# Kernel tuning notes

Hardware: AMD Instinct MI355X
Metric: run time of the kernel (lower is better)

Reference implementation:

```python
import jax, jax.numpy as jnp
import numpy as np

B, N, DIM, VDIM, H, HD = 4, 1369, 1024, 1536, 16, 64
ROPE_HW, ROPE_DIM, THETA = 37, 32, 10000.0
LN_EPS = 1e-5


def _rope_tables():
    # VisionRotaryEmbeddingFast: freqs_for='lang', dim=32, pt_seq_len=ft_seq_len=37
    inv = 1.0 / THETA ** (jnp.arange(0, ROPE_DIM, 2, dtype=jnp.float32) / ROPE_DIM)  # [16]
    t = jnp.arange(ROPE_HW, dtype=jnp.float32) / ROPE_HW * ROPE_HW                    # [37]
    f = t[:, None] * inv[None, :]                                                     # [37,16]
    f = jnp.repeat(f, 2, axis=-1)                                                     # [37,32]
    # broadcat along last dim over the 2D grid -> [37,37,64]
    f2 = jnp.concatenate([jnp.broadcast_to(f[:, None, :], (ROPE_HW, ROPE_HW, ROPE_DIM)),
                          jnp.broadcast_to(f[None, :, :], (ROPE_HW, ROPE_HW, ROPE_DIM))], axis=-1)
    f2 = f2.reshape(-1, 2 * ROPE_DIM)                                                 # [1369,64]
    return jnp.cos(f2), jnp.sin(f2)


def _rotate_half(x):
    # pairs (x0,x1) -> (-x1,x0), interleaved
    xr = x.reshape(*x.shape[:-1], x.shape[-1] // 2, 2)
    x1, x2 = xr[..., 0], xr[..., 1]
    return jnp.stack((-x2, x1), axis=-1).reshape(x.shape)


def setup_inputs() -> dict:
    key = jax.random.key(0)
    ks = jax.random.split(key, 8)
    return {
        "x": jax.random.normal(ks[0], (B, N, DIM), jnp.float32),
        "value": jax.random.normal(ks[1], (B, N, VDIM), jnp.float32),
        "attn_mask": jax.random.randint(ks[2], (B, N), 0, 2).astype(bool),
        "wq": jax.random.normal(ks[3], (DIM, DIM), jnp.float32) * 0.02,
        "wk": jax.random.normal(ks[4], (DIM, VDIM), jnp.float32) * 0.02,
        "wv": jax.random.normal(ks[5], (DIM, VDIM), jnp.float32) * 0.02,
        "ln_g": jnp.ones((DIM,), jnp.float32),
        "ln_b": jnp.zeros((DIM,), jnp.float32),
        "wp": jax.random.normal(ks[6], (DIM, DIM), jnp.float32) * 0.02,
        "bp": jnp.zeros((DIM,), jnp.float32),
    }


def reference(x, value, attn_mask, wq, wk, wv, ln_g, ln_b, wp, bp):
    cos, sin = _rope_tables()  # [N, 64] each
    # projections (torch F.linear: y = x @ W.T)
    q = jnp.einsum('bni,oi->bno', x, wq).reshape(B, N, H, HD).transpose(0, 2, 1, 3)
    k = jnp.einsum('bni,oi->bno', value, wk).reshape(B, N, H, HD).transpose(0, 2, 1, 3)
    v = jnp.einsum('bni,oi->bno', value, wv).reshape(B, N, H, HD).transpose(0, 2, 1, 3)
    # inline RoPE on q and k
    q = q * cos + _rotate_half(q) * sin
    k = k * cos + _rotate_half(k) * sin
    q = q * (HD ** -0.5)
    attn = jnp.einsum('bhnd,bhmd->bhnm', q, k)
    neg_inf = jnp.finfo(attn.dtype).min
    attn = jnp.where(attn_mask[:, None, None, :], attn, neg_inf)
    attn = jax.nn.softmax(attn, axis=-1)
    out = jnp.einsum('bhnm,bhmd->bhnd', attn, v)
    out = out.transpose(0, 2, 1, 3).reshape(B, N, H * HD)
    # inner_attn_ln (LayerNorm, eps=1e-5)
    mu = jnp.mean(out, axis=-1, keepdims=True)
    var = jnp.var(out, axis=-1, keepdims=True)
    out = (out - mu) * jax.lax.rsqrt(var + LN_EPS) * ln_g + ln_b
    # output projection
    return jnp.einsum('bni,oi->bno', out, wp) + bp
```

## Files before the change

kernel.cpp:

```cpp
#include <hip/hip_runtime.h>
#include <hip/hip_bf16.h>

#define BB 4
#define NN 1369
#define DIMM 1024
#define VDIMM 1536
#define HH 16
#define MM (BB*NN)
#define MPAD 5504
#define MPAD2 5632
#define NPAD 1408
#define KVB 64
#define NT (NPAD/KVB)
#define NT2 (NPAD/128)
#define QSCALE 0.18028334f

typedef __attribute__((ext_vector_type(4))) float f32x4;
typedef __attribute__((ext_vector_type(8))) __bf16 bf16x8;
typedef __attribute__((ext_vector_type(4))) __bf16 bf16x4;

#define GLOAD_LDS(gsrc, ldst) \
  __builtin_amdgcn_global_load_lds((const __attribute__((address_space(1))) unsigned int*)(gsrc), \
                                   (__attribute__((address_space(3))) unsigned int*)(ldst), 16, 0, 0)

__global__ __launch_bounds__(256) void cvt_inputs(const float* __restrict__ x,
                                                  const float* __restrict__ val,
                                                  __bf16* __restrict__ xb,
                                                  __bf16* __restrict__ vb) {
  const int NX = MM * 1024 / 4;
  const int NV = MM * 1536 / 4;
  int i = blockIdx.x * blockDim.x + threadIdx.x;
  int st = gridDim.x * blockDim.x;
  for (; i < NX + NV; i += st) {
    const float* s; __bf16* d; int j;
    if (i < NX) { s = x; d = xb; j = i; }
    else        { s = val; d = vb; j = i - NX; }
    f32x4 v = ((const f32x4*)s)[j];
    bf16x4 o;
    o[0] = (__bf16)v[0]; o[1] = (__bf16)v[1];
    o[2] = (__bf16)v[2]; o[3] = (__bf16)v[3];
    ((bf16x4*)d)[j] = o;
  }
}

__global__ __launch_bounds__(256) void cvt_weights(
    const float* __restrict__ wq, const float* __restrict__ wk,
    const float* __restrict__ wv, const float* __restrict__ wp,
    const float* __restrict__ g,
    __bf16* __restrict__ wqb, __bf16* __restrict__ wkvb, __bf16* __restrict__ wgb) {
  const int NQ = 1024 * 1024 / 4;
  const int NK = 1024 * 1536 / 4;
  int i = blockIdx.x * blockDim.x + threadIdx.x;
  int st = gridDim.x * blockDim.x;
  for (; i < 2 * NQ + 2 * NK; i += st) {
    int j = i;
    if (j < NQ) {
      f32x4 v = ((const f32x4*)wq)[j];
      bf16x4 o;
      o[0] = (__bf16)v[0]; o[1] = (__bf16)v[1]; o[2] = (__bf16)v[2]; o[3] = (__bf16)v[3];
      ((bf16x4*)wqb)[j] = o;
    } else if (j < NQ + NK) {
      j -= NQ;
      f32x4 v = ((const f32x4*)wk)[j];
      bf16x4 o;
      o[0] = (__bf16)v[0]; o[1] = (__bf16)v[1]; o[2] = (__bf16)v[2]; o[3] = (__bf16)v[3];
      ((bf16x4*)wkvb)[j] = o;
    } else if (j < NQ + 2 * NK) {
      j -= NQ + NK;
      f32x4 v = ((const f32x4*)wv)[j];
      bf16x4 o;
      o[0] = (__bf16)v[0]; o[1] = (__bf16)v[1]; o[2] = (__bf16)v[2]; o[3] = (__bf16)v[3];
      ((bf16x4*)(wkvb + (size_t)1024 * 1536))[j] = o;
    } else {
      j -= NQ + 2 * NK;
      f32x4 v = ((const f32x4*)wp)[j];
      f32x4 gv = ((const f32x4*)g)[j & 255];
      bf16x4 o;
      o[0] = (__bf16)(v[0] * gv[0]); o[1] = (__bf16)(v[1] * gv[1]);
      o[2] = (__bf16)(v[2] * gv[2]); o[3] = (__bf16)(v[3] * gv[3]);
      ((bf16x4*)wgb)[j] = o;
    }
  }
}

__global__ __launch_bounds__(256) void c12_kernel(
    const float* __restrict__ wp, const float* __restrict__ g,
    const float* __restrict__ lnb, const float* __restrict__ bpv,
    float* __restrict__ c1, float* __restrict__ c2) {
  const int w = threadIdx.x >> 6, l = threadIdx.x & 63;
  const int o = blockIdx.x * 4 + w;
  const float* row = wp + (size_t)o * 1024;
  float s1 = 0.f, s2 = 0.f;
#pragma unroll
  for (int j = 0; j < 4; ++j) {
    const int idx = l * 4 + j * 256;
    f32x4 wv = *(const f32x4*)&row[idx];
    f32x4 gv = *(const f32x4*)&g[idx];
    f32x4 bv = *(const f32x4*)&lnb[idx];
#pragma unroll
    for (int e = 0; e < 4; ++e) { s1 += wv[e] * gv[e]; s2 += wv[e] * bv[e]; }
  }
#pragma unroll
  for (int m = 1; m < 64; m <<= 1) { s1 += __shfl_xor(s1, m); s2 += __shfl_xor(s2, m); }
  if (l == 0) { c1[o] = s1; c2[o] = s2 + bpv[o]; }
}

__global__ __launch_bounds__(256) void stats_kernel(
    const __bf16* __restrict__ AO, float* __restrict__ mu, float* __restrict__ rstd) {
  const int w = threadIdx.x >> 6, l = threadIdx.x & 63;
  const int row = blockIdx.x * 4 + w;
  const __bf16* x = AO + (size_t)row * DIMM + l * 16;
  float s = 0.f, sq = 0.f;
#pragma unroll
  for (int j = 0; j < 2; ++j) {
    bf16x8 v = *(const bf16x8*)&x[j * 8];
#pragma unroll
    for (int e = 0; e < 8; ++e) { float f = (float)v[e]; s += f; sq += f * f; }
  }
#pragma unroll
  for (int m = 1; m < 64; m <<= 1) { s += __shfl_xor(s, m); sq += __shfl_xor(sq, m); }
  if (l == 0) {
    float mean = s * (1.f / 1024.f);
    mu[row] = mean;
    rstd[row] = rsqrtf(sq * (1.f / 1024.f) - mean * mean + 1e-5f);
  }
}

__global__ __launch_bounds__(256) void prep_aux(float* __restrict__ cosT,
                                                float* __restrict__ sinT,
                                                const void* __restrict__ mask,
                                                float* __restrict__ maskA) {
  const int blk = blockIdx.x;
  if (blk < 343) {
    int idx = blk * 256 + threadIdx.x;
    if (idx >= NN * 64) return;
    int n = idx >> 6, d = idx & 63;
    int r = n / 37, c = n % 37;
    int m = (d < 32) ? (d >> 1) : ((d - 32) >> 1);
    float p = (d < 32) ? (float)r : (float)c;
    float inv = powf(10000.f, -(float)m * (1.f / 16.f));
    float a = p * inv;
    cosT[idx] = cosf(a);
    sinT[idx] = sinf(a);
  } else {
    __shared__ int flags[2];
    int t = threadIdx.x;
    if (t < 2) flags[t] = 0;
    __syncthreads();
    const unsigned int* mw = (const unsigned int*)mask;
    for (int i = t; i < NN; i += blockDim.x) {
      unsigned int w = mw[i];
      if (w == 0x3F800000u) atomicOr(&flags[1], 1);
      else if (w > 1u) atomicOr(&flags[0], 1);
    }
    __syncthreads();
    int md = flags[1] ? 2 : (flags[0] ? 1 : 0);
    const unsigned char* mb = (const unsigned char*)mask;
    const float* mf = (const float*)mask;
    for (int i = t; i < BB * NPAD; i += blockDim.x) {
      int b = i / NPAD, key = i % NPAD;
      float v = -1e30f;
      if (key < NN) {
        int idx = b * NN + key;
        bool on = (md == 0) ? (mw[idx] != 0u) : (md == 1) ? (mb[idx] != 0) : (mf[idx] != 0.f);
        if (on) v = 0.f;
      }
      maskA[i] = v;
    }
  }
}

__global__ __launch_bounds__(512, 2) void gemm_kv256(
    const __bf16* __restrict__ A, const __bf16* __restrict__ W,
    __bf16* __restrict__ Kb, __bf16* __restrict__ Vtb,
    const float* __restrict__ cosT, const float* __restrict__ sinT) {
  __shared__ __bf16 Ar[4][256 * 32];
  __shared__ __bf16 Br[4][256 * 32];
  const int tid = threadIdx.x;
  const int wid = tid >> 6, l = tid & 63;
  const int wr = wid >> 2, wc = wid & 3;
  const int lo = l & 15, hi = l >> 4;
  const int tN = blockIdx.x & 7, tM = blockIdx.x >> 3;
  const int K = VDIMM;
  const int nk = K / 32;

  const int srow = (tid >> 6) * 16 + (tid & 15);
  const int schunk = ((tid >> 4) & 3) * 8;
  const __bf16* Asrc = A + (size_t)(tM * 256 + srow) * K + schunk;
  const __bf16* Wsrc = W + (size_t)(tN * 256 + srow) * K + schunk;

  f32x4 zero = {0.f, 0.f, 0.f, 0.f};
  f32x4 acc[8][4];
#pragma unroll
  for (int i = 0; i < 8; ++i)
#pragma unroll
    for (int j = 0; j < 4; ++j) acc[i][j] = zero;

  auto GSTAGE = [&](int s, int k0) {
    GLOAD_LDS(Asrc + k0,                   (char*)&Ar[s][0] + tid * 16);
    GLOAD_LDS(Asrc + (size_t)128 * K + k0, (char*)&Ar[s][0] + tid * 16 + 8192);
    GLOAD_LDS(Wsrc + k0,                   (char*)&Br[s][0] + tid * 16);
    GLOAD_LDS(Wsrc + (size_t)128 * K + k0, (char*)&Br[s][0] + tid * 16 + 8192);
  };

  GSTAGE(0, 0);
  GSTAGE(1, 32);
  for (int t = 0; t < nk; ++t) {
    if (t < nk - 1) asm volatile("s_waitcnt vmcnt(4)" ::: "memory");
    else            asm volatile("s_waitcnt vmcnt(0)" ::: "memory");
    __builtin_amdgcn_s_barrier();
    const int s = t & 3;
    bf16x8 af[8], bf[4];
#pragma unroll
    for (int mi = 0; mi < 8; ++mi)
      af[mi] = *(const bf16x8*)&Ar[s][(wr * 8 + mi) * 512 + hi * 128 + lo * 8];
#pragma unroll
    for (int ni = 0; ni < 4; ++ni)
      bf[ni] = *(const bf16x8*)&Br[s][(wc * 4 + ni) * 512 + hi * 128 + lo * 8];
    if (t + 2 < nk) GSTAGE((t + 2) & 3, (t + 2) * 32);
    __builtin_amdgcn_s_setprio(1);
#pragma unroll
    for (int mi = 0; mi < 8; ++mi)
#pragma unroll
      for (int ni = 0; ni < 4; ++ni)
        acc[mi][ni] = __builtin_amdgcn_mfma_f32_16x16x32_bf16(af[mi], bf[ni], acc[mi][ni], 0, 0, 0);
    __builtin_amdgcn_s_setprio(0);
  }

  const int m_base = tM * 256 + wr * 128;
  const int o_base = tN * 256 + wc * 64;
  const bool isK = (tN < 4);
#pragma unroll
  for (int mi = 0; mi < 8; ++mi) {
    const int m4 = m_base + mi * 16 + hi * 4;
    if (!isK) {
      if (m4 < MM) {
        const int b0 = m4 / NN, n0 = m4 % NN;
#pragma unroll
        for (int ni = 0; ni < 4; ++ni) {
          const int o2 = o_base + ni * 16 + lo - 1024;
          const int h = o2 >> 6, d = o2 & 63;
          if (n0 <= NN - 4) {
            bf16x4 pv;
#pragma unroll
            for (int r = 0; r < 4; ++r) pv[r] = (__bf16)acc[mi][ni][r];
            *(bf16x4*)&Vtb[((size_t)(b0 * HH + h) * 64 + d) * NPAD + n0] = pv;
          } else {
#pragma unroll
            for (int r = 0; r < 4; ++r) {
              const int mr = m4 + r;
              const int br = mr / NN, nr = mr % NN;
              Vtb[((size_t)(br * HH + h) * 64 + d) * NPAD + nr] = (__bf16)acc[mi][ni][r];
            }
          }
        }
      }
    } else {
#pragma unroll
      for (int r = 0; r < 4; ++r) {
        const int mrow = m4 + r;
#pragma unroll
        for (int ni = 0; ni < 4; ++ni) {
          const int col = o_base + ni * 16 + lo;
          float v = acc[mi][ni][r];
          float pprt = __shfl_xor(v, 1);
          if (mrow < MM) {
            int b = mrow / NN, n = mrow % NN;
            int h = col >> 6, d = col & 63;
            float cs = cosT[n * 64 + d], sn = sinT[n * 64 + d];
            float out = v * cs + (((d & 1) == 0) ? -pprt : pprt) * sn;
            Kb[((size_t)(b * HH + h) * NPAD + n) * 64 + d] = (__bf16)out;
          }
        }
      }
    }
  }
}

template <int EPI>
__global__ __launch_bounds__(256) void gemm_bt(
    const __bf16* __restrict__ A, const __bf16* __restrict__ W, int K,
    __bf16* __restrict__ obf, float* __restrict__ of32,
    const float* __restrict__ cosT, const float* __restrict__ sinT,
    const float* __restrict__ mu, const float* __restrict__ rstd,
    const float* __restrict__ c1, const float* __restrict__ c2) {
  __shared__ __bf16 As[2][128 * 32];
  __shared__ __bf16 Bs[2][64 * 32];
  const int tid = threadIdx.x;
  const int w = tid >> 6, l = tid & 63;
  const int tN = blockIdx.x, tM = blockIdx.y;
  const int wmo = w * 32;
  const int lo = l & 15, hi = l >> 4;

  const __bf16* Asrc = A + (size_t)(tM * 128 + lo) * K + hi * 8;
  const __bf16* Wsrc = W + (size_t)(tN * 64 + lo) * K + hi * 8;

  f32x4 zero = {0.f, 0.f, 0.f, 0.f};
  f32x4 acc[2][4];
#pragma unroll
  for (int i = 0; i < 2; ++i)
#pragma unroll
    for (int j = 0; j < 4; ++j) acc[i][j] = zero;

  auto GSTAGE = [&](int buf, int k0) {
#pragma unroll
    for (int j = 0; j < 2; ++j) {
      const int c = j * 4 + w;
      GLOAD_LDS(Asrc + (size_t)c * 16 * K + k0, (char*)&As[buf][c * 512]);
    }
    GLOAD_LDS(Wsrc + (size_t)w * 16 * K + k0, (char*)&Bs[buf][w * 512]);
  };

  const int nk = K >> 5;
  GSTAGE(0, 0);
  int cur = 0;
  const int ga = wmo >> 4;
  for (int t = 0; t < nk; ++t) {
    __syncthreads();
    if (t + 1 < nk) GSTAGE(cur ^ 1, (t + 1) * 32);
    bf16x8 af[2], bfr[4];
#pragma unroll
    for (int mi = 0; mi < 2; ++mi)
      af[mi] = *(const bf16x8*)&As[cur][(ga + mi) * 512 + hi * 128 + lo * 8];
#pragma unroll
    for (int ni = 0; ni < 4; ++ni)
      bfr[ni] = *(const bf16x8*)&Bs[cur][ni * 512 + hi * 128 + lo * 8];
    __builtin_amdgcn_s_setprio(1);
#pragma unroll
    for (int mi = 0; mi < 2; ++mi)
#pragma unroll
      for (int ni = 0; ni < 4; ++ni)
        acc[mi][ni] = __builtin_amdgcn_mfma_f32_16x16x32_bf16(af[mi], bfr[ni], acc[mi][ni], 0, 0, 0);
    __builtin_amdgcn_s_setprio(0);
    cur ^= 1;
  }

  const int m_base = tM * 128 + wmo;
  const int o_base = tN * 64;
  float c1v[4], c2v[4];
  if (EPI == 3) {
#pragma unroll
    for (int ni = 0; ni < 4; ++ni) {
      c1v[ni] = c1[o_base + ni * 16 + lo];
      c2v[ni] = c2[o_base + ni * 16 + lo];
    }
  }
#pragma unroll
  for (int mi = 0; mi < 2; ++mi) {
#pragma unroll
    for (int r = 0; r < 4; ++r) {
      const int mrow = m_base + mi * 16 + hi * 4 + r;
#pragma unroll
      for (int ni = 0; ni < 4; ++ni) {
        const int col = o_base + ni * 16 + lo;
        float v = acc[mi][ni][r];
        if (EPI == 0) {
          float pprt = __shfl_xor(v, 1);
          if (mrow < MM) {
            int b = mrow / NN, n = mrow % NN;
            int h = col >> 6, d = col & 63;
            float cs = cosT[n * 64 + d], sn = sinT[n * 64 + d];
            float out = (v * cs + (((d & 1) == 0) ? -pprt : pprt) * sn) * QSCALE;
            obf[((size_t)(b * HH + h) * NPAD + n) * 64 + d] = (__bf16)out;
          }
        } else {
          if (mrow < MM)
            of32[(size_t)mrow * DIMM + col] =
                rstd[mrow] * (v - mu[mrow] * c1v[ni]) + c2v[ni];
        }
      }
    }
  }
}

__device__ inline unsigned int pk2(float a, float b) {
  unsigned int ua = (unsigned int)__builtin_bit_cast(unsigned short, (__bf16)a);
  unsigned int ub = (unsigned int)__builtin_bit_cast(unsigned short, (__bf16)b);
  return ua | (ub << 16);
}

__global__ __launch_bounds__(256) void attn_kernel(
    const __bf16* __restrict__ Qb, const __bf16* __restrict__ Kb,
    const __bf16* __restrict__ Vtb, const float* __restrict__ maskA,
    __bf16* __restrict__ AO) {
  __shared__ __bf16 Ks[2][64 * 64];
  __shared__ __bf16 Vs[2][64 * 64];
  __shared__ unsigned int Plds[4][32 * 32];
  const int tid = threadIdx.x;
  const int w = tid >> 6, l = tid & 63;
  const int lo = l & 15, hi = l >> 4;

  const int i = blockIdx.x;
  const int orig = (i & 7) * 88 + (i >> 3);
  const int bh = orig / NT2;
  const int qt = orig % NT2;
  const int b = bh >> 4;
  const int q0 = qt * 128 + w * 32;

  const __bf16* Qp = Qb + ((size_t)bh * NPAD + q0) * 64;
  bf16x8 qf0a = *(const bf16x8*)&Qp[lo * 64 + hi * 8];
  bf16x8 qf1a = *(const bf16x8*)&Qp[lo * 64 + 32 + hi * 8];
  bf16x8 qf0b = *(const bf16x8*)&Qp[(16 + lo) * 64 + hi * 8];
  bf16x8 qf1b = *(const bf16x8*)&Qp[(16 + lo) * 64 + 32 + hi * 8];

  const int row8 = l >> 3;
  const int swz16 = ((l & 7) ^ row8) << 4;
  const int lo7 = lo & 7;
  const int swzW = (lo & 7) << 2;

  f32x4 zero = {0.f, 0.f, 0.f, 0.f};
  f32x4 O[4][2];
#pragma unroll
  for (int n = 0; n < 4; ++n) { O[n][0] = zero; O[n][1] = zero; }
  float lr[2] = {0.f, 0.f};
  const float* mk = maskA + b * NPAD;

#define STAGE(buf, k0)                                                                   \
  {                                                                                      \
    _Pragma("unroll") for (int j = 0; j < 2; ++j) {                                      \
      const int rbase = (j * 4 + w) * 8;                                                 \
      const char* ksrc = (const char*)Kb +                                               \
          ((size_t)bh * NPAD + (k0) + rbase + row8) * 128 + swz16;                       \
      GLOAD_LDS(ksrc, (char*)&Ks[buf][0] + rbase * 128);                                 \
      const char* vsrc = (const char*)Vtb +                                              \
          ((size_t)(bh * 64 + rbase + row8) * NPAD + (k0)) * 2 + swz16;                  \
      GLOAD_LDS(vsrc, (char*)&Vs[buf][0] + rbase * 128);                                 \
    }                                                                                    \
  }

  STAGE(0, 0);
  __syncthreads();
  int cur = 0;

  for (int t = 0; t < NT; ++t) {
    if (t + 1 < NT) STAGE(cur ^ 1, (t + 1) * KVB);

    const __bf16* KB = &Ks[cur][0];
    const __bf16* VB = &Vs[cur][0];

    f32x4 mv[4];
#pragma unroll
    for (int c = 0; c < 4; ++c) mv[c] = *(const f32x4*)&mk[t * KVB + c * 16 + hi * 4];

    f32x4 S[4][2];
    __builtin_amdgcn_s_setprio(1);
#pragma unroll
    for (int c = 0; c < 4; ++c) {
      const int kr = c * 16 + lo;
      bf16x8 kfa = *(const bf16x8*)&KB[kr * 64 + ((hi ^ lo7) * 8)];
      bf16x8 kfb = *(const bf16x8*)&KB[kr * 64 + (((hi + 4) ^ lo7) * 8)];
      f32x4 sa = __builtin_amdgcn_mfma_f32_16x16x32_bf16(kfa, qf0a, zero, 0, 0, 0);
      S[c][0]   = __builtin_amdgcn_mfma_f32_16x16x32_bf16(kfb, qf1a, sa, 0, 0, 0);
      f32x4 sb = __builtin_amdgcn_mfma_f32_16x16x32_bf16(kfa, qf0b, zero, 0, 0, 0);
      S[c][1]   = __builtin_amdgcn_mfma_f32_16x16x32_bf16(kfb, qf1b, sb, 0, 0, 0);
    }
    __builtin_amdgcn_s_setprio(0);

#pragma unroll
    for (int qb = 0; qb < 2; ++qb) {
      float rs = 0.f;
#pragma unroll
      for (int c = 0; c < 4; ++c) {
        float p0 = exp2f(S[c][qb][0] + mv[c][0]);
        float p1 = exp2f(S[c][qb][1] + mv[c][1]);
        float p2 = exp2f(S[c][qb][2] + mv[c][2]);
        float p3 = exp2f(S[c][qb][3] + mv[c][3]);
        rs += (p0 + p1) + (p2 + p3);
        uint2 pw = {pk2(p0, p1), pk2(p2, p3)};
        *(uint2*)&Plds[w][(qb * 16 + lo) * 32 + ((8 * c + 2 * hi) ^ swzW)] = pw;
      }
      lr[qb] += rs;
    }

    bf16x8 pf0a = *(const bf16x8*)&Plds[w][lo * 32 + ((4 * hi) ^ swzW)];
    bf16x8 pf1a = *(const bf16x8*)&Plds[w][lo * 32 + ((16 + 4 * hi) ^ swzW)];
    bf16x8 pf0b = *(const bf16x8*)&Plds[w][(16 + lo) * 32 + ((4 * hi) ^ swzW)];
    bf16x8 pf1b = *(const bf16x8*)&Plds[w][(16 + lo) * 32 + ((16 + 4 * hi) ^ swzW)];

    __builtin_amdgcn_s_setprio(1);
#pragma unroll
    for (int n = 0; n < 4; ++n) {
      const int vr = n * 16 + lo;
      bf16x8 vfa = *(const bf16x8*)&VB[vr * 64 + ((hi ^ lo7) * 8)];
      bf16x8 vfb = *(const bf16x8*)&VB[vr * 64 + (((hi + 4) ^ lo7) * 8)];
      O[n][0] = __builtin_amdgcn_mfma_f32_16x16x32_bf16(vfa, pf0a, O[n][0], 0, 0, 0);
      O[n][0] = __builtin_amdgcn_mfma_f32_16x16x32_bf16(vfb, pf1a, O[n][0], 0, 0, 0);
      O[n][1] = __builtin_amdgcn_mfma_f32_16x16x32_bf16(vfa, pf0b, O[n][1], 0, 0, 0);
      O[n][1] = __builtin_amdgcn_mfma_f32_16x16x32_bf16(vfb, pf1b, O[n][1], 0, 0, 0);
    }
    __builtin_amdgcn_s_setprio(0);

    __syncthreads();
    cur ^= 1;
  }
#undef STAGE

  const int h = bh & 15;
#pragma unroll
  for (int qb = 0; qb < 2; ++qb) {
    float s = lr[qb];
    s += __shfl_xor(s, 16);
    s += __shfl_xor(s, 32);
    const float inv = 1.f / s;
    const int token = q0 + qb * 16 + lo;
    if (token < NN) {
      __bf16* dst = AO + (size_t)(b * NN + token) * DIMM + h * 64 + hi * 4;
#pragma unroll
      for (int n = 0; n < 4; ++n) {
        bf16x4 o;
#pragma unroll
        for (int e = 0; e < 4; ++e) o[e] = (__bf16)(O[n][qb][e] * inv);
        *(bf16x4*)(dst + n * 16) = o;
      }
    }
  }
}

extern "C" void kernel_launch(void* const* d_in, const int* in_sizes, int n_in,
                              void* d_out, int out_size, void* d_ws, size_t ws_size,
                              hipStream_t stream) {
  const float* x   = (const float*)d_in[0];
  const float* val = (const float*)d_in[1];
  const void*  msk = d_in[2];
  const float* wq  = (const float*)d_in[3];
  const float* wk  = (const float*)d_in[4];
  const float* wv  = (const float*)d_in[5];
  const float* lng = (const float*)d_in[6];
  const float* lnb = (const float*)d_in[7];
  const float* wp  = (const float*)d_in[8];
  const float* bpv = (const float*)d_in[9];
  float* out = (float*)d_out;

  char* ws = (char*)d_ws;
  size_t off = 0;
  auto alloc = [&](size_t bytes) -> char* {
    char* p = ws + off;
    off += (bytes + 255) & ~(size_t)255;
    return p;
  };
  __bf16* xb   = (__bf16*)alloc((size_t)MPAD * 1024 * 2);
  __bf16* vb   = (__bf16*)alloc((size_t)MPAD2 * 1536 * 2);
  __bf16* wqb  = (__bf16*)alloc((size_t)1024 * 1024 * 2);
  __bf16* wkvb = (__bf16*)alloc((size_t)2048 * 1536 * 2);
  __bf16* wgb  = (__bf16*)alloc((size_t)1024 * 1024 * 2);
  __bf16* Qb   = (__bf16*)alloc((size_t)64 * NPAD * 64 * 2);
  __bf16* Kb   = (__bf16*)alloc((size_t)64 * NPAD * 64 * 2);
  __bf16* Vtb  = (__bf16*)alloc((size_t)64 * 64 * NPAD * 2);
  __bf16* AO   = (__bf16*)alloc((size_t)MPAD * 1024 * 2);
  float* cosT  = (float*)alloc((size_t)NN * 64 * 4);
  float* sinT  = (float*)alloc((size_t)NN * 64 * 4);
  float* maskA = (float*)alloc((size_t)BB * NPAD * 4);
  float* muv   = (float*)alloc((size_t)MM * 4);
  float* rstdv = (float*)alloc((size_t)MM * 4);
  float* c1v   = (float*)alloc((size_t)1024 * 4);
  float* c2v   = (float*)alloc((size_t)1024 * 4);


  cvt_inputs<<<2048, 256, 0, stream>>>(x, val, xb, vb);
  cvt_weights<<<1024, 256, 0, stream>>>(wq, wk, wv, wp, lng, wqb, wkvb, wgb);
  prep_aux<<<344, 256, 0, stream>>>(cosT, sinT, msk, maskA);
  c12_kernel<<<256, 256, 0, stream>>>(wp, lng, lnb, bpv, c1v, c2v);

  gemm_bt<0><<<dim3(16, 43), 256, 0, stream>>>(xb, wqb, 1024, Qb, nullptr,
                                               cosT, sinT, nullptr, nullptr, nullptr, nullptr);
  gemm_kv256<<<dim3(176), 512, 0, stream>>>(vb, wkvb, Kb, Vtb, cosT, sinT);

  attn_kernel<<<dim3(64 * NT2), 256, 0, stream>>>(Qb, Kb, Vtb, maskA, AO);

  stats_kernel<<<MM / 4, 256, 0, stream>>>(AO, muv, rstdv);

  gemm_bt<3><<<dim3(16, 43), 256, 0, stream>>>(AO, wgb, 1024, nullptr, out,
                                               nullptr, nullptr, muv, rstdv, c1v, c2v);
}
```

Measured before the change: 263.0 us.

## Merge Q and KV projection GEMMs into one launch with XCD-partitioned tiles

Replaces the separate Q projection GEMM launch and the 256x256-tile KV GEMM with a single kernel whose blocks are split by XCD index: two XCDs compute Q tiles (128x64, RoPE plus scale) and six compute KV tiles (128x128, double-buffered). This removes one launch and lets the Q and KV work run concurrently, filling the GPU better than 176 large blocks. In exchange it drops the 4-stage pipeline and large-tile reuse of the old KV kernel, and it depends on an assumed round-robin block-to-XCD mapping for load balance.

```diff
diff --git a/kernel.cpp b/kernel.cpp
--- a/kernel.cpp
+++ b/kernel.cpp
@@ -8,7 +8,6 @@
 #define HH 16
 #define MM (BB*NN)
 #define MPAD 5504
-#define MPAD2 5632
 #define NPAD 1408
 #define KVB 64
 #define NT (NPAD/KVB)
@@ -170,95 +169,74 @@
   }
 }
 
-__global__ __launch_bounds__(512, 2) void gemm_kv256(
-    const __bf16* __restrict__ A, const __bf16* __restrict__ W,
-    __bf16* __restrict__ Kb, __bf16* __restrict__ Vtb,
+__global__ __launch_bounds__(256) void gemm_qkv2(
+    const __bf16* __restrict__ xb, const __bf16* __restrict__ wqb,
+    const __bf16* __restrict__ vb, const __bf16* __restrict__ wkvb,
+    __bf16* __restrict__ Qb, __bf16* __restrict__ Kb, __bf16* __restrict__ Vtb,
     const float* __restrict__ cosT, const float* __restrict__ sinT) {
-  __shared__ __bf16 Ar[4][256 * 32];
-  __shared__ __bf16 Br[4][256 * 32];
+  __shared__ __bf16 As[2][128 * 32];
+  __shared__ __bf16 Bs[2][128 * 32];
   const int tid = threadIdx.x;
-  const int wid = tid >> 6, l = tid & 63;
-  const int wr = wid >> 2, wc = wid & 3;
+  const int w = tid >> 6, l = tid & 63;
+  const int bid = blockIdx.x;
+  const int xcd = bid & 7, slot = bid >> 3;
   const int lo = l & 15, hi = l >> 4;
-  const int tN = blockIdx.x & 7, tM = blockIdx.x >> 3;
-  const int K = VDIMM;
-  const int nk = K / 32;
-
-  const int srow = (tid >> 6) * 16 + (tid & 15);
-  const int schunk = ((tid >> 4) & 3) * 8;
-  const __bf16* Asrc = A + (size_t)(tM * 256 + srow) * K + schunk;
-  const __bf16* Wsrc = W + (size_t)(tN * 256 + srow) * K + schunk;
-
   f32x4 zero = {0.f, 0.f, 0.f, 0.f};
-  f32x4 acc[8][4];
-#pragma unroll
-  for (int i = 0; i < 8; ++i)
-#pragma unroll
-    for (int j = 0; j < 4; ++j) acc[i][j] = zero;
-
-  auto GSTAGE = [&](int s, int k0) {
-    GLOAD_LDS(Asrc + k0,                   (char*)&Ar[s][0] + tid * 16);
-    GLOAD_LDS(Asrc + (size_t)128 * K + k0, (char*)&Ar[s][0] + tid * 16 + 8192);
-    GLOAD_LDS(Wsrc + k0,                   (char*)&Br[s][0] + tid * 16);
-    GLOAD_LDS(Wsrc + (size_t)128 * K + k0, (char*)&Br[s][0] + tid * 16 + 8192);
-  };
-
-  GSTAGE(0, 0);
-  GSTAGE(1, 32);
-  for (int t = 0; t < nk; ++t) {
-    if (t < nk - 1) asm volatile("s_waitcnt vmcnt(4)" ::: "memory");
-    else            asm volatile("s_waitcnt vmcnt(0)" ::: "memory");
-    __builtin_amdgcn_s_barrier();
-    const int s = t & 3;
-    bf16x8 af[8], bf[4];
-#pragma unroll
-    for (int mi = 0; mi < 8; ++mi)
-      af[mi] = *(const bf16x8*)&Ar[s][(wr * 8 + mi) * 512 + hi * 128 + lo * 8];
-#pragma unroll
-    for (int ni = 0; ni < 4; ++ni)
-      bf[ni] = *(const bf16x8*)&Br[s][(wc * 4 + ni) * 512 + hi * 128 + lo * 8];
-    if (t + 2 < nk) GSTAGE((t + 2) & 3, (t + 2) * 32);
-    __builtin_amdgcn_s_setprio(1);
-#pragma unroll
-    for (int mi = 0; mi < 8; ++mi)
+
+  if (xcd < 2) {
+    const int qid = xcd * 344 + slot;
+    const int tN = qid & 15, tM = qid >> 4;
+    const int K = 1024;
+    const int wmo = w * 32;
+
+    const __bf16* Asrc = xb + (size_t)(tM * 128 + lo) * K + hi * 8;
+    const __bf16* Wsrc = wqb + (size_t)(tN * 64 + lo) * K + hi * 8;
+
+    f32x4 acc[2][4];
+#pragma unroll
+    for (int i = 0; i < 2; ++i)
+#pragma unroll
+      for (int j = 0; j < 4; ++j) acc[i][j] = zero;
+
+    auto GSTAGE = [&](int buf, int k0) {
+#pragma unroll
+      for (int j = 0; j < 2; ++j) {
+        const int c = j * 4 + w;
+        GLOAD_LDS(Asrc + (size_t)c * 16 * K + k0, (char*)&As[buf][c * 512]);
+      }
+      GLOAD_LDS(Wsrc + (size_t)w * 16 * K + k0, (char*)&Bs[buf][w * 512]);
+    };
+
+    GSTAGE(0, 0);
+    int cur = 0;
+    const int ga = wmo >> 4;
+    for (int t = 0; t < 32; ++t) {
+      __syncthreads();
+      if (t + 1 < 32) GSTAGE(cur ^ 1, (t + 1) * 32);
+      bf16x8 af[2], bfr[4];
+#pragma unroll
+      for (int mi = 0; mi < 2; ++mi)
+        af[mi] = *(const bf16x8*)&As[cur][(ga + mi) * 512 + hi * 128 + lo * 8];
 #pragma unroll
       for (int ni = 0; ni < 4; ++ni)
-        acc[mi][ni] = __builtin_amdgcn_mfma_f32_16x16x32_bf16(af[mi], bf[ni], acc[mi][ni], 0, 0, 0);
-    __builtin_amdgcn_s_setprio(0);
-  }
-
-  const int m_base = tM * 256 + wr * 128;
-  const int o_base = tN * 256 + wc * 64;
-  const bool isK = (tN < 4);
-#pragma unroll
-  for (int mi = 0; mi < 8; ++mi) {
-    const int m4 = m_base + mi * 16 + hi * 4;
-    if (!isK) {
-      if (m4 < MM) {
-        const int b0 = m4 / NN, n0 = m4 % NN;
-#pragma unroll
-        for (int ni = 0; ni < 4; ++ni) {
-          const int o2 = o_base + ni * 16 + lo - 1024;
-          const int h = o2 >> 6, d = o2 & 63;
-          if (n0 <= NN - 4) {
-            bf16x4 pv;
-#pragma unroll
-            for (int r = 0; r < 4; ++r) pv[r] = (__bf16)acc[mi][ni][r];
-            *(bf16x4*)&Vtb[((size_t)(b0 * HH + h) * 64 + d) * NPAD + n0] = pv;
-          } else {
-#pragma unroll
-            for (int r = 0; r < 4; ++r) {
-              const int mr = m4 + r;
-              const int br = mr / NN, nr = mr % NN;
-              Vtb[((size_t)(br * HH + h) * 64 + d) * NPAD + nr] = (__bf16)acc[mi][ni][r];
-            }
-          }
-        }
-      }
-    } else {
+        bfr[ni] = *(const bf16x8*)&Bs[cur][ni * 512 + hi * 128 + lo * 8];
+      __builtin_amdgcn_s_setprio(1);
+#pragma unroll
+      for (int mi = 0; mi < 2; ++mi)
+#pragma unroll
+        for (int ni = 0; ni < 4; ++ni)
+          acc[mi][ni] = __builtin_amdgcn_mfma_f32_16x16x32_bf16(af[mi], bfr[ni], acc[mi][ni], 0, 0, 0);
+      __builtin_amdgcn_s_setprio(0);
+      cur ^= 1;
+    }
+
+    const int m_base = tM * 128 + wmo;
+    const int o_base = tN * 64;
+#pragma unroll
+    for (int mi = 0; mi < 2; ++mi) {
 #pragma unroll
       for (int r = 0; r < 4; ++r) {
-        const int mrow = m4 + r;
+        const int mrow = m_base + mi * 16 + hi * 4 + r;
 #pragma unroll
         for (int ni = 0; ni < 4; ++ni) {
           const int col = o_base + ni * 16 + lo;
@@ -268,8 +246,106 @@
             int b = mrow / NN, n = mrow % NN;
             int h = col >> 6, d = col & 63;
             float cs = cosT[n * 64 + d], sn = sinT[n * 64 + d];
-            float out = v * cs + (((d & 1) == 0) ? -pprt : pprt) * sn;
-            Kb[((size_t)(b * HH + h) * NPAD + n) * 64 + d] = (__bf16)out;
+            float out = (v * cs + (((d & 1) == 0) ? -pprt : pprt) * sn) * QSCALE;
+            Qb[((size_t)(b * HH + h) * NPAD + n) * 64 + d] = (__bf16)out;
+          }
+        }
+      }
+    }
+  } else {
+    const int kvid = (xcd - 2) * 115 + slot;
+    if (kvid >= 688) return;
+    const int tN = kvid & 15, tM = kvid >> 4;
+    const int K = VDIMM;
+    const int wm = w >> 1, wn = w & 1;
+    const int wmo = wm * 64;
+
+    const __bf16* Asrc = vb + (size_t)(tM * 128 + lo) * K + hi * 8;
+    const __bf16* Wsrc = wkvb + (size_t)(tN * 128 + lo) * K + hi * 8;
+
+    f32x4 acc[4][4];
+#pragma unroll
+    for (int i = 0; i < 4; ++i)
+#pragma unroll
+      for (int j = 0; j < 4; ++j) acc[i][j] = zero;
+
+    auto GSTAGE = [&](int buf, int k0) {
+#pragma unroll
+      for (int j = 0; j < 2; ++j) {
+        const int c = j * 4 + w;
+        GLOAD_LDS(Asrc + (size_t)c * 16 * K + k0, (char*)&As[buf][c * 512]);
+        GLOAD_LDS(Wsrc + (size_t)c * 16 * K + k0, (char*)&Bs[buf][c * 512]);
+      }
+    };
+
+    GSTAGE(0, 0);
+    int cur = 0;
+    const int ga = wmo >> 4;
+    const int gb = wn * 4;
+    for (int t = 0; t < 48; ++t) {
+      __syncthreads();
+      if (t + 1 < 48) GSTAGE(cur ^ 1, (t + 1) * 32);
+      bf16x8 af[4], bfr[4];
+#pragma unroll
+      for (int mi = 0; mi < 4; ++mi)
+        af[mi] = *(const bf16x8*)&As[cur][(ga + mi) * 512 + hi * 128 + lo * 8];
+#pragma unroll
+      for (int ni = 0; ni < 4; ++ni)
+        bfr[ni] = *(const bf16x8*)&Bs[cur][(gb + ni) * 512 + hi * 128 + lo * 8];
+      __builtin_amdgcn_s_setprio(1);
+#pragma unroll
+      for (int mi = 0; mi < 4; ++mi)
+#pragma unroll
+        for (int ni = 0; ni < 4; ++ni)
+          acc[mi][ni] = __builtin_amdgcn_mfma_f32_16x16x32_bf16(af[mi], bfr[ni], acc[mi][ni], 0, 0, 0);
+      __builtin_amdgcn_s_setprio(0);
+      cur ^= 1;
+    }
+
+    const int m_base = tM * 128 + wmo;
+    const int o_base = tN * 128 + wn * 64;
+    const bool isK = (tN < 8);
+#pragma unroll
+    for (int mi = 0; mi < 4; ++mi) {
+      const int m4 = m_base + mi * 16 + hi * 4;
+      if (!isK) {
+        if (m4 < MM) {
+          const int b0 = m4 / NN, n0 = m4 % NN;
+#pragma unroll
+          for (int ni = 0; ni < 4; ++ni) {
+            const int o2 = o_base + ni * 16 + lo - 1024;
+            const int h = o2 >> 6, d = o2 & 63;
+            if (n0 <= NN - 4) {
+              bf16x4 pv;
+#pragma unroll
+              for (int r = 0; r < 4; ++r) pv[r] = (__bf16)acc[mi][ni][r];
+              *(bf16x4*)&Vtb[((size_t)(b0 * HH + h) * 64 + d) * NPAD + n0] = pv;
+            } else {
+#pragma unroll
+              for (int r = 0; r < 4; ++r) {
+                const int mr = m4 + r;
+                const int br = mr / NN, nr = mr % NN;
+                Vtb[((size_t)(br * HH + h) * 64 + d) * NPAD + nr] = (__bf16)acc[mi][ni][r];
+              }
+            }
+          }
+        }
+      } else {
+#pragma unroll
+        for (int r = 0; r < 4; ++r) {
+          const int mrow = m4 + r;
+#pragma unroll
+          for (int ni = 0; ni < 4; ++ni) {
+            const int col = o_base + ni * 16 + lo;
+            float v = acc[mi][ni][r];
+            float pprt = __shfl_xor(v, 1);
+            if (mrow < MM) {
+              int b = mrow / NN, n = mrow % NN;
+              int h = col >> 6, d = col & 63;
+              float cs = cosT[n * 64 + d], sn = sinT[n * 64 + d];
+              float out = v * cs + (((d & 1) == 0) ? -pprt : pprt) * sn;
+              Kb[((size_t)(b * HH + h) * NPAD + n) * 64 + d] = (__bf16)out;
+            }
           }
         }
       }
@@ -539,7 +615,7 @@
     return p;
   };
   __bf16* xb   = (__bf16*)alloc((size_t)MPAD * 1024 * 2);
-  __bf16* vb   = (__bf16*)alloc((size_t)MPAD2 * 1536 * 2);
+  __bf16* vb   = (__bf16*)alloc((size_t)MPAD * 1536 * 2);
   __bf16* wqb  = (__bf16*)alloc((size_t)1024 * 1024 * 2);
   __bf16* wkvb = (__bf16*)alloc((size_t)2048 * 1536 * 2);
   __bf16* wgb  = (__bf16*)alloc((size_t)1024 * 1024 * 2);
@@ -561,9 +637,7 @@
   prep_aux<<<344, 256, 0, stream>>>(cosT, sinT, msk, maskA);
   c12_kernel<<<256, 256, 0, stream>>>(wp, lng, lnb, bpv, c1v, c2v);
 
-  gemm_bt<0><<<dim3(16, 43), 256, 0, stream>>>(xb, wqb, 1024, Qb, nullptr,
-                                               cosT, sinT, nullptr, nullptr, nullptr, nullptr);
-  gemm_kv256<<<dim3(176), 512, 0, stream>>>(vb, wkvb, Kb, Vtb, cosT, sinT);
+  gemm_qkv2<<<dim3(2752), 256, 0, stream>>>(xb, wqb, vb, wkvb, Qb, Kb, Vtb, cosT, sinT);
 
   attn_kernel<<<dim3(64 * NT2), 256, 0, stream>>>(Qb, Kb, Vtb, maskA, AO);
 
```

New measurement: 453.6 us. 72.5% more time.

## Replace 256x256 KV GEMM with 128x128 double-buffered tiles and swizzled block order

Applied to the files above, without the earlier changes.

Swaps the K/V projection GEMM from 256x256 tiles (512 threads, 4-stage LDS ring, 176 blocks) to 128x128 tiles with 256 threads, double buffering and 688 blocks. Block indices are remapped so consecutive blocks are spread across tile positions, which may help L2 reuse or balance. The 176-block launch likely underfilled the GPU's compute units, and more blocks give better occupancy. The cost is lower per-block data reuse and a shallower prefetch pipeline.

```diff
diff --git a/kernel.cpp b/kernel.cpp
--- a/kernel.cpp
+++ b/kernel.cpp
@@ -8,7 +8,6 @@
 #define HH 16
 #define MM (BB*NN)
 #define MPAD 5504
-#define MPAD2 5632
 #define NPAD 1408
 #define KVB 64
 #define NT (NPAD/KVB)
@@ -170,68 +169,70 @@
   }
 }
 
-__global__ __launch_bounds__(512, 2) void gemm_kv256(
+__global__ __launch_bounds__(256) void gemm_kv(
     const __bf16* __restrict__ A, const __bf16* __restrict__ W,
     __bf16* __restrict__ Kb, __bf16* __restrict__ Vtb,
     const float* __restrict__ cosT, const float* __restrict__ sinT) {
-  __shared__ __bf16 Ar[4][256 * 32];
-  __shared__ __bf16 Br[4][256 * 32];
+  __shared__ __bf16 As[2][128 * 32];
+  __shared__ __bf16 Bs[2][128 * 32];
   const int tid = threadIdx.x;
-  const int wid = tid >> 6, l = tid & 63;
-  const int wr = wid >> 2, wc = wid & 3;
+  const int w = tid >> 6, l = tid & 63;
+  const int i0 = blockIdx.x;
+  const int orig = (i0 & 7) * 86 + (i0 >> 3);
+  const int tN = orig & 15, tM = orig >> 4;
+  const int K = VDIMM;
+  const int wm = w >> 1, wn = w & 1;
+  const int wmo = wm * 64;
   const int lo = l & 15, hi = l >> 4;
-  const int tN = blockIdx.x & 7, tM = blockIdx.x >> 3;
-  const int K = VDIMM;
-  const int nk = K / 32;
-
-  const int srow = (tid >> 6) * 16 + (tid & 15);
-  const int schunk = ((tid >> 4) & 3) * 8;
-  const __bf16* Asrc = A + (size_t)(tM * 256 + srow) * K + schunk;
-  const __bf16* Wsrc = W + (size_t)(tN * 256 + srow) * K + schunk;
+
+  const __bf16* Asrc = A + (size_t)(tM * 128 + lo) * K + hi * 8;
+  const __bf16* Wsrc = W + (size_t)(tN * 128 + lo) * K + hi * 8;
 
   f32x4 zero = {0.f, 0.f, 0.f, 0.f};
-  f32x4 acc[8][4];
-#pragma unroll
-  for (int i = 0; i < 8; ++i)
+  f32x4 acc[4][4];
+#pragma unroll
+  for (int i = 0; i < 4; ++i)
 #pragma unroll
     for (int j = 0; j < 4; ++j) acc[i][j] = zero;
 
-  auto GSTAGE = [&](int s, int k0) {
-    GLOAD_LDS(Asrc + k0,                   (char*)&Ar[s][0] + tid * 16);
-    GLOAD_LDS(Asrc + (size_t)128 * K + k0, (char*)&Ar[s][0] + tid * 16 + 8192);
-    GLOAD_LDS(Wsrc + k0,                   (char*)&Br[s][0] + tid * 16);
-    GLOAD_LDS(Wsrc + (size_t)128 * K + k0, (char*)&Br[s][0] + tid * 16 + 8192);
+  auto GSTAGE = [&](int buf, int k0) {
+#pragma unroll
+    for (int j = 0; j < 2; ++j) {
+      const int c = j * 4 + w;
+      GLOAD_LDS(Asrc + (size_t)c * 16 * K + k0, (char*)&As[buf][c * 512]);
+      GLOAD_LDS(Wsrc + (size_t)c * 16 * K + k0, (char*)&Bs[buf][c * 512]);
+    }
   };
 
   GSTAGE(0, 0);
-  GSTAGE(1, 32);
-  for (int t = 0; t < nk; ++t) {
-    if (t < nk - 1) asm volatile("s_waitcnt vmcnt(4)" ::: "memory");
-    else            asm volatile("s_waitcnt vmcnt(0)" ::: "memory");
-    __builtin_amdgcn_s_barrier();
-    const int s = t & 3;
-    bf16x8 af[8], bf[4];
-#pragma unroll
-    for (int mi = 0; mi < 8; ++mi)
-      af[mi] = *(const bf16x8*)&Ar[s][(wr * 8 + mi) * 512 + hi * 128 + lo * 8];
+  int cur = 0;
+  const int ga = wmo >> 4;
+  const int gb = wn * 4;
+  for (int t = 0; t < 48; ++t) {
+    __syncthreads();
+    if (t + 1 < 48) GSTAGE(cur ^ 1, (t + 1) * 32);
+    bf16x8 af[4], bfr[4];
+#pragma unroll
+    for (int mi = 0; mi < 4; ++mi)
+      af[mi] = *(const bf16x8*)&As[cur][(ga + mi) * 512 + hi * 128 + lo * 8];
 #pragma unroll
     for (int ni = 0; ni < 4; ++ni)
-      bf[ni] = *(const bf16x8*)&Br[s][(wc * 4 + ni) * 512 + hi * 128 + lo * 8];
-    if (t + 2 < nk) GSTAGE((t + 2) & 3, (t + 2) * 32);
+      bfr[ni] = *(const bf16x8*)&Bs[cur][(gb + ni) * 512 + hi * 128 + lo * 8];
     __builtin_amdgcn_s_setprio(1);
 #pragma unroll
-    for (int mi = 0; mi < 8; ++mi)
+    for (int mi = 0; mi < 4; ++mi)
 #pragma unroll
       for (int ni = 0; ni < 4; ++ni)
-        acc[mi][ni] = __builtin_amdgcn_mfma_f32_16x16x32_bf16(af[mi], bf[ni], acc[mi][ni], 0, 0, 0);
+        acc[mi][ni] = __builtin_amdgcn_mfma_f32_16x16x32_bf16(af[mi], bfr[ni], acc[mi][ni], 0, 0, 0);
     __builtin_amdgcn_s_setprio(0);
-  }
-
-  const int m_base = tM * 256 + wr * 128;
-  const int o_base = tN * 256 + wc * 64;
-  const bool isK = (tN < 4);
-#pragma unroll
-  for (int mi = 0; mi < 8; ++mi) {
+    cur ^= 1;
+  }
+
+  const int m_base = tM * 128 + wmo;
+  const int o_base = tN * 128 + wn * 64;
+  const bool isK = (tN < 8);
+#pragma unroll
+  for (int mi = 0; mi < 4; ++mi) {
     const int m4 = m_base + mi * 16 + hi * 4;
     if (!isK) {
       if (m4 < MM) {
@@ -539,7 +540,7 @@
     return p;
   };
   __bf16* xb   = (__bf16*)alloc((size_t)MPAD * 1024 * 2);
-  __bf16* vb   = (__bf16*)alloc((size_t)MPAD2 * 1536 * 2);
+  __bf16* vb   = (__bf16*)alloc((size_t)MPAD * 1536 * 2);
   __bf16* wqb  = (__bf16*)alloc((size_t)1024 * 1024 * 2);
   __bf16* wkvb = (__bf16*)alloc((size_t)2048 * 1536 * 2);
   __bf16* wgb  = (__bf16*)alloc((size_t)1024 * 1024 * 2);
@@ -563,7 +564,7 @@
 
   gemm_bt<0><<<dim3(16, 43), 256, 0, stream>>>(xb, wqb, 1024, Qb, nullptr,
                                                cosT, sinT, nullptr, nullptr, nullptr, nullptr);
-  gemm_kv256<<<dim3(176), 512, 0, stream>>>(vb, wkvb, Kb, Vtb, cosT, sinT);
+  gemm_kv<<<dim3(688), 256, 0, stream>>>(vb, wkvb, Kb, Vtb, cosT, sinT);
 
   attn_kernel<<<dim3(64 * NT2), 256, 0, stream>>>(Qb, Kb, Vtb, maskA, AO);
 
```

Result: slower. 275.5 us (+4.8%).
